# Performance work log

Hardware: AMD Instinct MI355X
Metric: run time of the kernel (lower is better)

## Reference

```python
import jax, jax.numpy as jnp
import numpy as np

N = 100_000      # nodes
E = 1_600_000    # edges (avg degree 16)
IN_DIM = 165
HIDDEN = 64
OUT_DIM = 2


def setup_inputs() -> dict:
    key = jax.random.key(0)
    ks = jax.random.split(key, 10)
    x = jax.random.normal(ks[0], (N, IN_DIM), dtype=jnp.float32)
    edge_index = jax.random.randint(ks[1], (2, E), 0, N, dtype=jnp.int32)
    def lin(k, fan_in, fan_out):
        lim = 1.0 / np.sqrt(fan_in)
        return jax.random.uniform(k, (fan_in, fan_out), jnp.float32, -lim, lim)
    # SAGEConv: lin_l (neighbor path, with bias), lin_r (root path, no bias)
    W1l = lin(ks[2], IN_DIM, HIDDEN); b1 = jnp.zeros((HIDDEN,), jnp.float32)
    W1r = lin(ks[3], IN_DIM, HIDDEN)
    W2l = lin(ks[4], HIDDEN, HIDDEN); b2 = jnp.zeros((HIDDEN,), jnp.float32)
    W2r = lin(ks[5], HIDDEN, HIDDEN)
    Wc = lin(ks[6], HIDDEN, OUT_DIM)
    bc = jax.random.uniform(ks[7], (OUT_DIM,), jnp.float32, -0.1, 0.1)
    return {"x": x, "edge_index": edge_index, "W1l": W1l, "b1": b1, "W1r": W1r,
            "W2l": W2l, "b2": b2, "W2r": W2r, "Wc": Wc, "bc": bc}


def _sage_conv(h, src, dst, Wl, bl, Wr):
    # mean-aggregate source features at destination nodes, then two linears
    msg = h[src]                                              # [E, D] gather
    agg = jax.ops.segment_sum(msg, dst, num_segments=N)       # [N, D] scatter-add
    cnt = jax.ops.segment_sum(jnp.ones((src.shape[0], 1), h.dtype), dst,
                              num_segments=N)                 # [N, 1] in-degree
    mean = agg / jnp.maximum(cnt, 1.0)
    return mean @ Wl + bl + h @ Wr


def reference(x, edge_index, W1l, b1, W1r, W2l, b2, W2r, Wc, bc):
    src, dst = edge_index[0], edge_index[1]
    h = jax.nn.relu(_sage_conv(x, src, dst, W1l, b1, W1r))
    # dropout is a no-op at inference (training=False)
    h = jax.nn.relu(_sage_conv(h, src, dst, W2l, b2, W2r))
    return h @ Wc + bc
```

## Files before the change

kernel.cpp:

```cpp
#include <hip/hip_runtime.h>
#include <hip/hip_fp16.h>
#include <cstdint>

#define NN 100000
#define NE 1600000
#define INDIM 165
#define HID 64

constexpr int BSH = 7;
constexpr int BNODES = 128;
constexpr int NBUK = (NN + BNODES - 1) / BNODES;
constexpr int SC_CHUNK = 8192;


__global__ __launch_bounds__(256) void k_bhist(const int* __restrict__ dst,
                                               int* __restrict__ bhist, int ne) {
    __shared__ int h[NBUK];
    for (int b = threadIdx.x; b < NBUK; b += 256) h[b] = 0;
    __syncthreads();
    for (int e = blockIdx.x * blockDim.x + threadIdx.x; e < ne;
         e += gridDim.x * blockDim.x)
        atomicAdd(&h[dst[e] >> BSH], 1);
    __syncthreads();
    for (int b = threadIdx.x; b < NBUK; b += 256)
        if (h[b]) atomicAdd(&bhist[b], h[b]);
}


__global__ __launch_bounds__(256) void k_bscan(const int* __restrict__ bhist,
                                               int* __restrict__ bbase,
                                               int* __restrict__ bcursor) {
    __shared__ int wsum[4];
    const int tid = threadIdx.x, lane = tid & 63, wid = tid >> 6;
    int v[4];
    int tsum = 0;
#pragma unroll
    for (int i = 0; i < 4; ++i) {
        int idx = tid * 4 + i;
        v[i] = (idx < NBUK) ? bhist[idx] : 0;
        tsum += v[i];
    }
    int x = tsum;
#pragma unroll
    for (int off = 1; off < 64; off <<= 1) {
        int y = __shfl_up(x, off, 64);
        if (lane >= off) x += y;
    }
    if (lane == 63) wsum[wid] = x;
    __syncthreads();
    int woff = 0;
#pragma unroll
    for (int w = 0; w < 4; ++w)
        if (w < wid) woff += wsum[w];
    int run = woff + x - tsum;
#pragma unroll
    for (int i = 0; i < 4; ++i) {
        int idx = tid * 4 + i;
        if (idx < NBUK) { bbase[idx] = run; bcursor[idx] = run; }
        run += v[i];
    }
    if (tid == 255) bbase[NBUK] = woff + x;
}


__global__ __launch_bounds__(256) void k_scatter(const int* __restrict__ src,
                                                 const int* __restrict__ dst,
                                                 int* __restrict__ bcursor,
                                                 int2* __restrict__ E2, int ne) {
    __shared__ int hist[NBUK];
    __shared__ int base[NBUK];
    const int tid = threadIdx.x;
    const int cs = blockIdx.x * SC_CHUNK;
    for (int b = tid; b < NBUK; b += 256) hist[b] = 0;
    __syncthreads();
    unsigned pack[SC_CHUNK / 256];
#pragma unroll 8
    for (int i = 0; i < SC_CHUNK / 256; ++i) {
        int e = cs + i * 256 + tid;
        if (e < ne) {
            int b = dst[e] >> BSH;
            int r = atomicAdd(&hist[b], 1);
            pack[i] = (unsigned)((b << 13) | r);
        } else {
            pack[i] = 0xFFFFFFFFu;
        }
    }
    __syncthreads();
    for (int b = tid; b < NBUK; b += 256) {
        int c = hist[b];
        base[b] = c ? atomicAdd(&bcursor[b], c) : 0;
    }
    __syncthreads();
#pragma unroll 8
    for (int i = 0; i < SC_CHUNK / 256; ++i) {
        if (pack[i] != 0xFFFFFFFFu) {
            int e = cs + i * 256 + tid;
            int b = pack[i] >> 13, r = pack[i] & 8191;
            E2[base[b] + r] = make_int2(src[e], dst[e]);
        }
    }
}


__global__ __launch_bounds__(256) void k_csrb(const int2* __restrict__ E2,
                                              const int* __restrict__ bbase,
                                              int* __restrict__ rowptr,
                                              int* __restrict__ col, int n) {
    __shared__ int cnt[BNODES];
    __shared__ int pref[BNODES];
    const int tid = threadIdx.x;
    const int bs = bbase[blockIdx.x], be = bbase[blockIdx.x + 1];
    for (int i = tid; i < BNODES; i += 256) cnt[i] = 0;
    __syncthreads();
    for (int e = bs + tid; e < be; e += 256)
        atomicAdd(&cnt[E2[e].y & (BNODES - 1)], 1);
    __syncthreads();
    if (tid < 64) {
        int c0 = cnt[tid * 2], c1 = cnt[tid * 2 + 1];
        int s = c0 + c1;
        int x = s;
#pragma unroll
        for (int off = 1; off < 64; off <<= 1) {
            int y = __shfl_up(x, off, 64);
            if (tid >= off) x += y;
        }
        int ex = x - s;
        pref[tid * 2] = ex;
        pref[tid * 2 + 1] = ex + c0;
    }
    __syncthreads();
    const int nodeBase = blockIdx.x * BNODES;
    for (int i = tid; i < BNODES; i += 256) {
        int gn = nodeBase + i;
        if (gn < n) rowptr[gn] = bs + pref[i];
        cnt[i] = 0;
    }
    __syncthreads();
    for (int e = bs + tid; e < be; e += 256) {
        int2 pr = E2[e];
        int d = pr.y & (BNODES - 1);
        int r = atomicAdd(&cnt[d], 1);
        col[bs + pref[d] + r] = pr.x;
    }
    if (blockIdx.x == 0 && tid == 0) rowptr[n] = bbase[NBUK];
}


template <int K>
__global__ __launch_bounds__(256) void k_linear(const float* __restrict__ X,
                                                const float* __restrict__ Wl,
                                                const float* __restrict__ Wr,
                                                __half* __restrict__ Y,
                                                float* __restrict__ R, int n) {
    constexpr int KC = 32;
    constexpr int MT = 64;
    constexpr int LDX = 68;
    __shared__ float Xs[KC][LDX];
    __shared__ float Ws[KC][128];

    const int tid = threadIdx.x;
    const int m0 = (tid & 15) * 4;
    const int n0 = (tid >> 4) * 8;
    const int nodeBase = blockIdx.x * MT;

    float acc[4][8];
#pragma unroll
    for (int i = 0; i < 4; ++i)
#pragma unroll
        for (int j = 0; j < 8; ++j) acc[i][j] = 0.f;

    for (int c = 0; c < K; c += KC) {
        const int kw = (K - c < KC) ? (K - c) : KC;
        __syncthreads();
#pragma unroll
        for (int i = 0; i < 8; ++i) {
            int e = tid + i * 256;
            int k = e & 31;
            int m = e >> 5;
            int gn = nodeBase + m;
            if (gn >= n) gn = n - 1;
            Xs[k][m] = (k < kw) ? X[(size_t)gn * K + c + k] : 0.f;
        }
#pragma unroll
        for (int i = 0; i < 4; ++i) {
            int v = tid + i * 256;
            int k = v >> 5;
            int nf = (v & 31) * 4;
            float4 w;
            if (k < kw) {
                const float* sp = (nf < 64) ? (Wl + (size_t)(c + k) * HID + nf)
                                            : (Wr + (size_t)(c + k) * HID + (nf - 64));
                w = *(const float4*)sp;
            } else {
                w = make_float4(0.f, 0.f, 0.f, 0.f);
            }
            const int pos = ((nf >> 2) & 1) * 64 + (nf >> 3) * 4;
            *(float4*)&Ws[k][pos] = w;
        }
        __syncthreads();
#pragma unroll 4
        for (int kk = 0; kk < KC; ++kk) {
            const float4 xa = *(const float4*)&Xs[kk][m0];
            const float4 wa = *(const float4*)&Ws[kk][n0 >> 1];
            const float4 wb = *(const float4*)&Ws[kk][64 + (n0 >> 1)];
            const float xm[4] = {xa.x, xa.y, xa.z, xa.w};
            const float wn[8] = {wa.x, wa.y, wa.z, wa.w, wb.x, wb.y, wb.z, wb.w};
#pragma unroll
            for (int i = 0; i < 4; ++i)
#pragma unroll
                for (int j = 0; j < 8; ++j)
                    acc[i][j] = fmaf(xm[i], wn[j], acc[i][j]);
        }
    }

    if (n0 < HID) {
#pragma unroll
        for (int i = 0; i < 4; ++i) {
            const int gn = nodeBase + m0 + i;
            if (gn < n) {
                union { __half2 h2[4]; uint4 u4; } u;
#pragma unroll
                for (int q = 0; q < 4; ++q)
                    u.h2[q] = __float22half2_rn(
                        make_float2(acc[i][2 * q], acc[i][2 * q + 1]));
                *(uint4*)&Y[(size_t)gn * HID + n0] = u.u4;
            }
        }
    } else {
        const int nc = n0 - HID;
#pragma unroll
        for (int i = 0; i < 4; ++i) {
            const int gn = nodeBase + m0 + i;
            if (gn < n) {
                *(float4*)&R[(size_t)gn * HID + nc] =
                    make_float4(acc[i][0], acc[i][1], acc[i][2], acc[i][3]);
                *(float4*)&R[(size_t)gn * HID + nc + 4] =
                    make_float4(acc[i][4], acc[i][5], acc[i][6], acc[i][7]);
            }
        }
    }
}


template <bool CLS>
__global__ __launch_bounds__(256) void k_agg(const __half* __restrict__ Y,
                                             const float* __restrict__ Rm,
                                             const float* __restrict__ bias,
                                             const int* __restrict__ rowptr,
                                             const int* __restrict__ col,
                                             float* __restrict__ H,
                                             const float* __restrict__ Wc,
                                             const float* __restrict__ bc,
                                             float* __restrict__ out, int n) {
    const int lane = threadIdx.x & 63;
    const int node = blockIdx.x * 4 + (threadIdx.x >> 6);
    if (node >= n) return;
    const int half_ = lane >> 5;
    const int fl = (lane & 31) * 2;
    const int s = rowptr[node], e = rowptr[node + 1];
    float ax = 0.f, ay = 0.f;
    int i = s + half_;
    for (; i + 6 < e; i += 8) {
        int s0 = col[i], s1 = col[i + 2], s2 = col[i + 4], s3 = col[i + 6];
        float2 y0 = __half22float2(*(const __half2*)&Y[(size_t)s0 * HID + fl]);
        float2 y1 = __half22float2(*(const __half2*)&Y[(size_t)s1 * HID + fl]);
        float2 y2 = __half22float2(*(const __half2*)&Y[(size_t)s2 * HID + fl]);
        float2 y3 = __half22float2(*(const __half2*)&Y[(size_t)s3 * HID + fl]);
        ax += (y0.x + y1.x) + (y2.x + y3.x);
        ay += (y0.y + y1.y) + (y2.y + y3.y);
    }
    for (; i < e; i += 2) {
        float2 yv = __half22float2(*(const __half2*)&Y[(size_t)col[i] * HID + fl]);
        ax += yv.x;
        ay += yv.y;
    }
    ax += __shfl_xor(ax, 32, 64);
    ay += __shfl_xor(ay, 32, 64);
    const float vx = __shfl(ax, lane >> 1, 64);
    const float vy = __shfl(ay, lane >> 1, 64);
    const float acc = (lane & 1) ? vy : vx;
    const int deg = e - s;
    float h = acc / (float)(deg > 1 ? deg : 1) + bias[lane] + Rm[(size_t)node * HID + lane];
    h = fmaxf(h, 0.f);
    if (!CLS) {
        H[(size_t)node * HID + lane] = h;
    } else {
        float p0 = h * Wc[lane * 2 + 0];
        float p1 = h * Wc[lane * 2 + 1];
#pragma unroll
        for (int off = 32; off > 0; off >>= 1) {
            p0 += __shfl_xor(p0, off, 64);
            p1 += __shfl_xor(p1, off, 64);
        }
        if (lane == 0) {
            out[(size_t)node * 2 + 0] = p0 + bc[0];
            out[(size_t)node * 2 + 1] = p1 + bc[1];
        }
    }
}


extern "C" void kernel_launch(void* const* d_in, const int* in_sizes, int n_in,
                              void* d_out, int out_size, void* d_ws, size_t ws_size,
                              hipStream_t stream) {
    const float* x   = (const float*)d_in[0];
    const int*   ei  = (const int*)d_in[1];
    const float* W1l = (const float*)d_in[2];
    const float* b1  = (const float*)d_in[3];
    const float* W1r = (const float*)d_in[4];
    const float* W2l = (const float*)d_in[5];
    const float* b2  = (const float*)d_in[6];
    const float* W2r = (const float*)d_in[7];
    const float* Wc  = (const float*)d_in[8];
    const float* bc  = (const float*)d_in[9];
    float* out = (float*)d_out;
    const int* src = ei;
    const int* dst = ei + NE;

    char* base = (char*)d_ws;
    size_t off = 0;
    auto alloc = [&](size_t bytes) {
        void* p = base + off;
        off = (off + bytes + 255) & ~(size_t)255;
        return p;
    };
    int*    bhist   = (int*)alloc((size_t)NBUK * 4);
    int*    bbase   = (int*)alloc((size_t)(NBUK + 1) * 4);
    int*    bcursor = (int*)alloc((size_t)NBUK * 4);
    int*    rowptr  = (int*)alloc((size_t)(NN + 1) * 4);
    int*    col     = (int*)alloc((size_t)NE * 4);
    __half* Y       = (__half*)alloc((size_t)NN * HID * 2 + 256);
    float*  R       = (float*)alloc((size_t)NN * HID * 4);
    float*  H1      = (float*)alloc((size_t)NN * HID * 4);
    int2*   E2      = (int2*)Y;

    const int sb = (NE + SC_CHUNK - 1) / SC_CHUNK;

    hipMemsetAsync(bhist, 0, (size_t)NBUK * 4, stream);
    k_bhist<<<sb, 256, 0, stream>>>(dst, bhist, NE);
    k_bscan<<<1, 256, 0, stream>>>(bhist, bbase, bcursor);
    k_scatter<<<sb, 256, 0, stream>>>(src, dst, bcursor, E2, NE);
    k_csrb<<<NBUK, 256, 0, stream>>>(E2, bbase, rowptr, col, NN);

    k_linear<INDIM><<<(NN + 63) / 64, 256, 0, stream>>>(x, W1l, W1r, Y, R, NN);
    k_agg<false><<<(NN + 3) / 4, 256, 0, stream>>>(Y, R, b1, rowptr, col, H1,
                                                   nullptr, nullptr, nullptr, NN);
    k_linear<HID><<<(NN + 63) / 64, 256, 0, stream>>>(H1, W2l, W2r, Y, R, NN);
    k_agg<true><<<(NN + 3) / 4, 256, 0, stream>>>(Y, R, b2, rowptr, col, nullptr,
                                                  Wc, bc, out, NN);
}
```

Baseline: 382.1 us.

## Use fp16 MFMA matrix instructions for the SAGE linear projections

Replaces the scalar-FMA fp32 register-tiled GEMM in k_linear with MFMA 16x16x32 f16 instructions. Inputs and weights are converted to half precision when staged into shared memory, with transposed K-major layouts padded to 40. Each wave computes 16 nodes by 128 output columns, writing the neighbor path as fp16 and the root path as fp32. The aim is to cut ALU time in the dense projections, at the cost of fp16 rounding of x and the weights, which loses some accuracy.

Measured after the change: 408.3 us. 6.8% more time.

```diff
diff --git a/kernel.cpp b/kernel.cpp
--- a/kernel.cpp
+++ b/kernel.cpp
@@ -146,28 +146,31 @@
 }
 
 
+typedef _Float16 f16x8 __attribute__((ext_vector_type(8)));
+typedef float f32x4 __attribute__((ext_vector_type(4)));
+
 template <int K>
 __global__ __launch_bounds__(256) void k_linear(const float* __restrict__ X,
                                                 const float* __restrict__ Wl,
                                                 const float* __restrict__ Wr,
-                                                __half* __restrict__ Y,
+                                                _Float16* __restrict__ Y,
                                                 float* __restrict__ R, int n) {
     constexpr int KC = 32;
     constexpr int MT = 64;
-    constexpr int LDX = 68;
-    __shared__ float Xs[KC][LDX];
-    __shared__ float Ws[KC][128];
+    constexpr int LDK = 40;
+    __shared__ _Float16 Xs[MT][LDK];
+    __shared__ _Float16 Wt[128][LDK];
 
     const int tid = threadIdx.x;
-    const int m0 = (tid & 15) * 4;
-    const int n0 = (tid >> 4) * 8;
+    const int lane = tid & 63;
+    const int w = tid >> 6;
+    const int jn = lane & 15;
+    const int kq = lane >> 4;
     const int nodeBase = blockIdx.x * MT;
 
-    float acc[4][8];
-#pragma unroll
-    for (int i = 0; i < 4; ++i)
-#pragma unroll
-        for (int j = 0; j < 8; ++j) acc[i][j] = 0.f;
+    f32x4 acc[8];
+#pragma unroll
+    for (int t = 0; t < 8; ++t) acc[t] = (f32x4){0.f, 0.f, 0.f, 0.f};
 
     for (int c = 0; c < K; c += KC) {
         const int kw = (K - c < KC) ? (K - c) : KC;
@@ -175,68 +178,45 @@
 #pragma unroll
         for (int i = 0; i < 8; ++i) {
             int e = tid + i * 256;
-            int k = e & 31;
-            int m = e >> 5;
+            int k = e & 31, m = e >> 5;
             int gn = nodeBase + m;
             if (gn >= n) gn = n - 1;
-            Xs[k][m] = (k < kw) ? X[(size_t)gn * K + c + k] : 0.f;
-        }
-#pragma unroll
-        for (int i = 0; i < 4; ++i) {
+            float v = (k < kw) ? X[(size_t)gn * K + c + k] : 0.f;
+            Xs[m][k] = (_Float16)v;
+        }
+#pragma unroll
+        for (int i = 0; i < 16; ++i) {
             int v = tid + i * 256;
-            int k = v >> 5;
-            int nf = (v & 31) * 4;
-            float4 w;
-            if (k < kw) {
-                const float* sp = (nf < 64) ? (Wl + (size_t)(c + k) * HID + nf)
-                                            : (Wr + (size_t)(c + k) * HID + (nf - 64));
-                w = *(const float4*)sp;
-            } else {
-                w = make_float4(0.f, 0.f, 0.f, 0.f);
-            }
-            const int pos = ((nf >> 2) & 1) * 64 + (nf >> 3) * 4;
-            *(float4*)&Ws[k][pos] = w;
+            int col = v & 127, k = v >> 7;
+            float wv = 0.f;
+            if (k < kw)
+                wv = (col < HID) ? Wl[(size_t)(c + k) * HID + col]
+                                 : Wr[(size_t)(c + k) * HID + (col - HID)];
+            Wt[col][k] = (_Float16)wv;
         }
         __syncthreads();
-#pragma unroll 4
-        for (int kk = 0; kk < KC; ++kk) {
-            const float4 xa = *(const float4*)&Xs[kk][m0];
-            const float4 wa = *(const float4*)&Ws[kk][n0 >> 1];
-            const float4 wb = *(const float4*)&Ws[kk][64 + (n0 >> 1)];
-            const float xm[4] = {xa.x, xa.y, xa.z, xa.w};
-            const float wn[8] = {wa.x, wa.y, wa.z, wa.w, wb.x, wb.y, wb.z, wb.w};
-#pragma unroll
-            for (int i = 0; i < 4; ++i)
-#pragma unroll
-                for (int j = 0; j < 8; ++j)
-                    acc[i][j] = fmaf(xm[i], wn[j], acc[i][j]);
-        }
-    }
-
-    if (n0 < HID) {
-#pragma unroll
-        for (int i = 0; i < 4; ++i) {
-            const int gn = nodeBase + m0 + i;
-            if (gn < n) {
-                union { __half2 h2[4]; uint4 u4; } u;
-#pragma unroll
-                for (int q = 0; q < 4; ++q)
-                    u.h2[q] = __float22half2_rn(
-                        make_float2(acc[i][2 * q], acc[i][2 * q + 1]));
-                *(uint4*)&Y[(size_t)gn * HID + n0] = u.u4;
-            }
-        }
-    } else {
-        const int nc = n0 - HID;
-#pragma unroll
-        for (int i = 0; i < 4; ++i) {
-            const int gn = nodeBase + m0 + i;
-            if (gn < n) {
-                *(float4*)&R[(size_t)gn * HID + nc] =
-                    make_float4(acc[i][0], acc[i][1], acc[i][2], acc[i][3]);
-                *(float4*)&R[(size_t)gn * HID + nc + 4] =
-                    make_float4(acc[i][4], acc[i][5], acc[i][6], acc[i][7]);
-            }
+        const f16x8 xb = *(const f16x8*)&Xs[w * 16 + jn][kq * 8];
+#pragma unroll
+        for (int t = 0; t < 8; ++t) {
+            const f16x8 wa = *(const f16x8*)&Wt[t * 16 + jn][kq * 8];
+            acc[t] = __builtin_amdgcn_mfma_f32_16x16x32_f16(wa, xb, acc[t], 0, 0, 0);
+        }
+    }
+
+    const int gn = nodeBase + w * 16 + jn;
+    if (gn < n) {
+#pragma unroll
+        for (int t = 0; t < 4; ++t) {
+            const int cb = t * 16 + kq * 4;
+            union { _Float16 h[4]; uint2 u; } u;
+#pragma unroll
+            for (int r = 0; r < 4; ++r) u.h[r] = (_Float16)acc[t][r];
+            *(uint2*)&Y[(size_t)gn * HID + cb] = u.u;
+        }
+#pragma unroll
+        for (int t = 4; t < 8; ++t) {
+            const int cb = (t - 4) * 16 + kq * 4;
+            *(f32x4*)&R[(size_t)gn * HID + cb] = acc[t];
         }
     }
 }
@@ -342,10 +322,10 @@
     k_scatter<<<sb, 256, 0, stream>>>(src, dst, bcursor, E2, NE);
     k_csrb<<<NBUK, 256, 0, stream>>>(E2, bbase, rowptr, col, NN);
 
-    k_linear<INDIM><<<(NN + 63) / 64, 256, 0, stream>>>(x, W1l, W1r, Y, R, NN);
+    k_linear<INDIM><<<(NN + 63) / 64, 256, 0, stream>>>(x, W1l, W1r, (_Float16*)Y, R, NN);
     k_agg<false><<<(NN + 3) / 4, 256, 0, stream>>>(Y, R, b1, rowptr, col, H1,
                                                    nullptr, nullptr, nullptr, NN);
-    k_linear<HID><<<(NN + 63) / 64, 256, 0, stream>>>(H1, W2l, W2r, Y, R, NN);
+    k_linear<HID><<<(NN + 63) / 64, 256, 0, stream>>>(H1, W2l, W2r, (_Float16*)Y, R, NN);
     k_agg<true><<<(NN + 3) / 4, 256, 0, stream>>>(Y, R, b2, rowptr, col, nullptr,
                                                   Wc, bc, out, NN);
 }
```
